# Optimization experiments

Measured on AMD Instinct MI355X. Metric: run time of the kernel, lower is better.

Reference implementation:

```python
import jax, jax.numpy as jnp
import numpy as np

INPUT_SIZE = (320, 320)   # (ih, iw) from Detector.input_size
CONF_THRESH = 0.5
NMS_THRESH = 0.4
CLASS_OFFSET = 1e4        # class-offset trick: boxes of different classes never overlap,
                          # making joint NMS identical to the original per-class loop


def setup_inputs():
    key = jax.random.key(0)
    k1, k2, k3, k4 = jax.random.split(key, 4)
    B, N, C = 4, 6300, 80
    cxcy = jax.random.uniform(k1, (B, N, 2), dtype=jnp.float32) * 320.0
    wh = jax.random.uniform(k2, (B, N, 2), dtype=jnp.float32) * 120.0 + 4.0
    obj = jax.random.uniform(k3, (B, N, 1), dtype=jnp.float32)
    cls = jax.random.uniform(k4, (B, N, C), dtype=jnp.float32)
    prediction = jnp.concatenate([cxcy, wh, obj, cls], axis=-1)  # [B, N, 85]
    return {"prediction": prediction, "fh": 720, "fw": 1280}


def _pairwise_iou(b):
    # b: [N, 4] as (x1, y1, x2, y2); same +1 / eps convention as bbox_iou
    x1, y1, x2, y2 = b[:, 0], b[:, 1], b[:, 2], b[:, 3]
    iw = jnp.clip(jnp.minimum(x2[:, None], x2[None, :]) - jnp.maximum(x1[:, None], x1[None, :]) + 1, 0)
    ih = jnp.clip(jnp.minimum(y2[:, None], y2[None, :]) - jnp.maximum(y1[:, None], y1[None, :]) + 1, 0)
    inter = iw * ih
    area = (x2 - x1 + 1) * (y2 - y1 + 1)
    return inter / (area[:, None] + area[None, :] - inter + 1e-16)


def _nms_image(pred):
    # pred: [N, 85]
    N = pred.shape[0]
    obj = pred[:, 4]
    valid = obj >= CONF_THRESH                      # conf_thresh filter (as mask)
    cx, cy, w, h = pred[:, 0], pred[:, 1], pred[:, 2], pred[:, 3]
    boxes = jnp.stack([cx - w / 2, cy - h / 2, cx + w / 2, cy + h / 2], axis=1)
    class_conf = jnp.max(pred[:, 5:], axis=1)
    class_pred = jnp.argmax(pred[:, 5:], axis=1)
    # offset boxes per class -> cross-class IoU is exactly 0
    oboxes = boxes + (class_pred.astype(boxes.dtype) * CLASS_OFFSET)[:, None]
    score = jnp.where(valid, obj, -jnp.inf)
    order = jnp.argsort(-score)                     # descending confidence
    iou = _pairwise_iou(oboxes[order])              # [N, N]
    vs = valid[order]
    idx = jnp.arange(N)

    def step(sup, i):
        k = vs[i] & (~sup[i])                       # box i survives -> it suppresses
        sup = sup | (k & (idx > i) & (iou[i] >= NMS_THRESH))
        return sup, k

    _, keep_sorted = jax.lax.scan(step, jnp.zeros(N, dtype=bool), idx)
    keep = jnp.zeros(N, dtype=bool).at[order].set(keep_sorted)
    det = jnp.concatenate(
        [boxes, obj[:, None], class_conf[:, None], class_pred.astype(boxes.dtype)[:, None]],
        axis=1,
    )  # [N, 7] = (x1, y1, x2, y2, obj_conf, class_score, class_pred)
    return det, keep


def _bbox_fit(det, fh, fw):
    # det: [B, N, 7]; fh, fw python ints (frame size); INPUT_SIZE = (ih, iw)
    ih, iw = INPUT_SIZE
    fdim = max(fh, fw)
    pad_x = max((fh * iw / ih - fw) / 2, 0) * iw / fdim
    pad_y = max((fw * ih / iw - fh) / 2, 0) * ih / fdim
    sx = fw / (iw - 2 * pad_x)
    sy = fh / (ih - 2 * pad_y)
    x1 = jnp.clip((det[..., 0] - pad_x) * sx, 0, fw)
    y1 = jnp.clip((det[..., 1] - pad_y) * sy, 0, fh)
    x2 = jnp.clip((det[..., 2] - pad_x) * sx, 0, fw)
    y2 = jnp.clip((det[..., 3] - pad_y) * sy, 0, fh)
    return jnp.concatenate([jnp.stack([x1, y1, x2, y2], axis=-1), det[..., 4:]], axis=-1)


def reference(prediction, fh, fw):
    det, keep = jax.vmap(_nms_image)(prediction)    # [B, N, 7], [B, N]
    det = _bbox_fit(det, fh, fw)
    return det, keep
```

## Files before the change

### kernel.cpp

```cpp
#include <hip/hip_runtime.h>
#include <limits.h>
#include <math.h>

#define BB 4
#define NN 6300
#define NCLS 80
#define NB (BB * NCLS)
#define PSTRIDE 85
#define CONF_TH 0.5f
#define NMS_TH 0.4f
#define CAP2 512


__global__ void __launch_bounds__(320) zero_kernel(int* __restrict__ cnt_ws) {
  cnt_ws[threadIdx.x] = 0;
}

__global__ void __launch_bounds__(256) prep_kernel(
    const float* __restrict__ pred,
    const int* __restrict__ fhp, const int* __restrict__ fwp,
    float* __restrict__ det_out,
    float* __restrict__ keep_out,
    int*   __restrict__ cnt_ws,
    float* __restrict__ rec_ws)
{
  int gid = blockIdx.x * blockDim.x + threadIdx.x;
  if (gid >= BB * NN) return;
  const float* p = pred + (long)gid * PSTRIDE;

  float cx = p[0], cy = p[1], w = p[2], h = p[3], obj = p[4];
  float x1 = cx - 0.5f * w;
  float y1 = cy - 0.5f * h;
  float x2 = cx + 0.5f * w;
  float y2 = cy + 0.5f * h;

  float cmax = p[5];
  int cidx = 0;
  for (int j = 1; j < NCLS; ++j) {
    float v = p[5 + j];
    if (v > cmax) { cmax = v; cidx = j; }
  }

  double fh = (double)fhp[0], fw = (double)fwp[0];
  const double ihd = 320.0, iwd = 320.0;
  double fdim = fmax(fh, fw);
  double pad_x_d = fmax((fh * iwd / ihd - fw) / 2.0, 0.0) * iwd / fdim;
  double pad_y_d = fmax((fw * ihd / iwd - fh) / 2.0, 0.0) * ihd / fdim;
  float sx = (float)(fw / (iwd - 2.0 * pad_x_d));
  float sy = (float)(fh / (ihd - 2.0 * pad_y_d));
  float px = (float)pad_x_d, py = (float)pad_y_d;
  float fwf = (float)fw, fhf = (float)fh;

  float* d = det_out + (long)gid * 7;
  d[0] = fminf(fmaxf((x1 - px) * sx, 0.0f), fwf);
  d[1] = fminf(fmaxf((y1 - py) * sy, 0.0f), fhf);
  d[2] = fminf(fmaxf((x2 - px) * sx, 0.0f), fwf);
  d[3] = fminf(fmaxf((y2 - py) * sy, 0.0f), fhf);
  d[4] = obj;
  d[5] = cmax;
  d[6] = (float)cidx;

  keep_out[gid] = 0.0f;

  if (obj >= CONF_TH) {
    int b = gid / NN;
    int n = gid - b * NN;
    int bucket = b * NCLS + cidx;
    int pos = atomicAdd(&cnt_ws[bucket], 1);
    if (pos < CAP2) {
      float off = (float)cidx * 10000.0f;
      float* r = rec_ws + ((size_t)bucket * CAP2 + pos) * 6;
      r[0] = x1 + off;
      r[1] = y1 + off;
      r[2] = x2 + off;
      r[3] = y2 + off;
      r[4] = obj;
      r[5] = __int_as_float(n);
    }
  }
}

__global__ void __launch_bounds__(256) nms_kernel(
    const int*   __restrict__ cnt_ws,
    const float* __restrict__ rec_ws,
    float* __restrict__ keep_out)
{
  const int tid = threadIdx.x;
  const int wv = tid >> 6;
  const int lane = tid & 63;
  const int bucket0 = blockIdx.x * 4;

  {
    const int bucket = bucket0 + wv;
    const int cnt = min(cnt_ws[bucket], CAP2);
    if (cnt > 0 && cnt <= 64) {
      float x1 = 0.f, y1 = 0.f, x2 = 0.f, y2 = 0.f;
      int n = 0;
      unsigned long long key;
      if (lane < cnt) {
        const float* r = rec_ws + ((size_t)bucket * CAP2 + lane) * 6;
        x1 = r[0]; y1 = r[1]; x2 = r[2]; y2 = r[3];
        float sc = r[4];
        n = __float_as_int(r[5]);
        key = ((unsigned long long)__float_as_uint(sc) << 32) |
              (unsigned)(0x7FFFFFFF - n);
      } else {
        key = (unsigned long long)lane;
      }
      int src = lane;

      for (int k = 2; k <= 64; k <<= 1) {
        for (int j = k >> 1; j > 0; j >>= 1) {
          unsigned long long ok = __shfl_xor(key, j);
          int osrc = __shfl_xor(src, j);
          bool lower = ((lane & j) == 0);
          bool asc = ((lane & k) != 0);
          bool mine_gt = key > ok;
          bool take = asc ? (lower ? mine_gt : !mine_gt)
                          : (lower ? !mine_gt : mine_gt);
          if (take) { key = ok; src = osrc; }
        }
      }

      float sx1 = __shfl(x1, src), sy1 = __shfl(y1, src);
      float sx2 = __shfl(x2, src), sy2 = __shfl(y2, src);
      int   sn  = __shfl(n, src);
      float area = __fmul_rn(__fadd_rn(__fsub_rn(sx2, sx1), 1.0f),
                             __fadd_rn(__fsub_rn(sy2, sy1), 1.0f));

      unsigned long long sup = 0ull;
      for (int i = 0; i < cnt; ++i) {
        if ((sup >> i) & 1ull) continue;
        float bx1 = __shfl(sx1, i), by1 = __shfl(sy1, i);
        float bx2 = __shfl(sx2, i), by2 = __shfl(sy2, i);
        float bar = __shfl(area, i);
        bool kill = false;
        if (lane > i && lane < cnt) {
          float iw_ = fmaxf(__fadd_rn(__fsub_rn(fminf(bx2, sx2),
                                                fmaxf(bx1, sx1)), 1.0f), 0.0f);
          float ih_ = fmaxf(__fadd_rn(__fsub_rn(fminf(by2, sy2),
                                                fmaxf(by1, sy1)), 1.0f), 0.0f);
          float inter = __fmul_rn(iw_, ih_);
          float denom = __fadd_rn(__fsub_rn(__fadd_rn(bar, area), inter), 1e-16f);
          kill = __fdiv_rn(inter, denom) >= NMS_TH;
        }
        sup |= __ballot(kill);
      }
      if (lane < cnt && !((sup >> lane) & 1ull)) {
        int b = bucket / NCLS;
        keep_out[b * NN + sn] = 1.0f;
      }
    }
  }

  __syncthreads();

  __shared__ float s_sc[CAP2];
  __shared__ float s_x1[CAP2], s_y1[CAP2], s_x2[CAP2], s_y2[CAP2];
  __shared__ int   s_idx[CAP2];
  __shared__ unsigned char s_sup[CAP2];

  for (int w2 = 0; w2 < 4; ++w2) {
    const int bucket = bucket0 + w2;
    const int cnt = min(cnt_ws[bucket], CAP2);
    if (cnt <= 64) continue;

    for (int i = tid; i < cnt; i += 256) {
      const float* r = rec_ws + ((size_t)bucket * CAP2 + i) * 6;
      s_x1[i] = r[0]; s_y1[i] = r[1]; s_x2[i] = r[2]; s_y2[i] = r[3];
      s_sc[i] = r[4]; s_idx[i] = __float_as_int(r[5]);
      s_sup[i] = 0;
    }
    __syncthreads();

    int M = 1;
    while (M < cnt) M <<= 1;
    for (int i = cnt + tid; i < M; i += 256) {
      s_sc[i] = -INFINITY; s_idx[i] = INT_MAX;
      s_x1[i] = 0.f; s_y1[i] = 0.f; s_x2[i] = 0.f; s_y2[i] = 0.f;
    }
    __syncthreads();

    for (int k = 2; k <= M; k <<= 1) {
      for (int j = k >> 1; j > 0; j >>= 1) {
        for (int i = tid; i < M; i += 256) {
          int ixj = i ^ j;
          if (ixj > i) {
            float si = s_sc[i], sj = s_sc[ixj];
            int ii = s_idx[i], ij = s_idx[ixj];
            bool before_ij = (si > sj) || (si == sj && ii < ij);
            bool before_ji = (sj > si) || (sj == si && ij < ii);
            bool up = ((i & k) == 0);
            bool dosw = up ? before_ji : before_ij;
            if (dosw) {
              s_sc[i] = sj;  s_sc[ixj] = si;
              s_idx[i] = ij; s_idx[ixj] = ii;
              float t;
              t = s_x1[i]; s_x1[i] = s_x1[ixj]; s_x1[ixj] = t;
              t = s_y1[i]; s_y1[i] = s_y1[ixj]; s_y1[ixj] = t;
              t = s_x2[i]; s_x2[i] = s_x2[ixj]; s_x2[ixj] = t;
              t = s_y2[i]; s_y2[i] = s_y2[ixj]; s_y2[ixj] = t;
            }
          }
        }
        __syncthreads();
      }
    }

    const int b = bucket / NCLS;
    for (int i = 0; i < cnt; ++i) {
      if (!s_sup[i]) {
        float x1i = s_x1[i], y1i = s_y1[i], x2i = s_x2[i], y2i = s_y2[i];
        float ai = __fmul_rn(__fadd_rn(__fsub_rn(x2i, x1i), 1.0f),
                             __fadd_rn(__fsub_rn(y2i, y1i), 1.0f));
        if (tid == 0) keep_out[b * NN + s_idx[i]] = 1.0f;
        for (int j = i + 1 + tid; j < cnt; j += 256) {
          float iw_ = fmaxf(__fadd_rn(__fsub_rn(fminf(x2i, s_x2[j]),
                                                fmaxf(x1i, s_x1[j])), 1.0f), 0.0f);
          float ih_ = fmaxf(__fadd_rn(__fsub_rn(fminf(y2i, s_y2[j]),
                                                fmaxf(y1i, s_y1[j])), 1.0f), 0.0f);
          float inter = __fmul_rn(iw_, ih_);
          float aj = __fmul_rn(__fadd_rn(__fsub_rn(s_x2[j], s_x1[j]), 1.0f),
                               __fadd_rn(__fsub_rn(s_y2[j], s_y1[j]), 1.0f));
          float denom = __fadd_rn(__fsub_rn(__fadd_rn(ai, aj), inter), 1e-16f);
          if (__fdiv_rn(inter, denom) >= NMS_TH) s_sup[j] = 1;
        }
      }
      __syncthreads();
    }
    __syncthreads();
  }
}

extern "C" void kernel_launch(void* const* d_in, const int* in_sizes, int n_in,
                              void* d_out, int out_size, void* d_ws, size_t ws_size,
                              hipStream_t stream) {
  const float* pred = (const float*)d_in[0];
  const int* fhp = (const int*)d_in[1];
  const int* fwp = (const int*)d_in[2];

  float* det_out  = (float*)d_out;
  float* keep_out = det_out + (size_t)BB * NN * 7;

  int*   cnt_ws = (int*)d_ws;
  float* rec_ws = (float*)((char*)d_ws + 4096);

  zero_kernel<<<1, NB, 0, stream>>>(cnt_ws);

  int nThreads = BB * NN;
  prep_kernel<<<(nThreads + 255) / 256, 256, 0, stream>>>(
      pred, fhp, fwp, det_out, keep_out, cnt_ws, rec_ws);

  nms_kernel<<<NB / 4, 256, 0, stream>>>(cnt_ws, rec_ws, keep_out);
}
```

Baseline: 84.50 us.

## Fuse zero, prep and NMS kernels into one launch with grid barriers

Replaces the three separate kernel launches (counter zeroing, box prep and bucketing, per-class NMS) with a single 99-block kernel. Block 0 clears the counters and publishes a magic flag that the other blocks wait on, and an atomic arrival counter acts as a grid barrier before the first 80 blocks run NMS. This removes two launch gaps and the inter-kernel idle time. In exchange it relies on all blocks being resident at the same time for the spin-waits. The flag is never reset between calls, so later invocations may start bucketing before block 0 has cleared the counters.

After: 95.25 us. 1.13x slower.

```diff
diff --git a/kernel.cpp b/kernel.cpp
--- a/kernel.cpp
+++ b/kernel.cpp
@@ -10,85 +10,113 @@
 #define CONF_TH 0.5f
 #define NMS_TH 0.4f
 #define CAP2 512
-
-
-__global__ void __launch_bounds__(320) zero_kernel(int* __restrict__ cnt_ws) {
-  cnt_ws[threadIdx.x] = 0;
-}
-
-__global__ void __launch_bounds__(256) prep_kernel(
+#define NBLK 99
+#define NMSBLK 80
+#define MAGIC 0x51D3C0DE
+
+
+__global__ void __launch_bounds__(256) fused_kernel(
     const float* __restrict__ pred,
     const int* __restrict__ fhp, const int* __restrict__ fwp,
     float* __restrict__ det_out,
     float* __restrict__ keep_out,
-    int*   __restrict__ cnt_ws,
+    int*   ctrl,
     float* __restrict__ rec_ws)
 {
-  int gid = blockIdx.x * blockDim.x + threadIdx.x;
-  if (gid >= BB * NN) return;
-  const float* p = pred + (long)gid * PSTRIDE;
-
-  float cx = p[0], cy = p[1], w = p[2], h = p[3], obj = p[4];
-  float x1 = cx - 0.5f * w;
-  float y1 = cy - 0.5f * h;
-  float x2 = cx + 0.5f * w;
-  float y2 = cy + 0.5f * h;
-
-  float cmax = p[5];
-  int cidx = 0;
-  for (int j = 1; j < NCLS; ++j) {
-    float v = p[5 + j];
-    if (v > cmax) { cmax = v; cidx = j; }
-  }
-
-  double fh = (double)fhp[0], fw = (double)fwp[0];
-  const double ihd = 320.0, iwd = 320.0;
-  double fdim = fmax(fh, fw);
-  double pad_x_d = fmax((fh * iwd / ihd - fw) / 2.0, 0.0) * iwd / fdim;
-  double pad_y_d = fmax((fw * ihd / iwd - fh) / 2.0, 0.0) * ihd / fdim;
-  float sx = (float)(fw / (iwd - 2.0 * pad_x_d));
-  float sy = (float)(fh / (ihd - 2.0 * pad_y_d));
-  float px = (float)pad_x_d, py = (float)pad_y_d;
-  float fwf = (float)fw, fhf = (float)fh;
-
-  float* d = det_out + (long)gid * 7;
-  d[0] = fminf(fmaxf((x1 - px) * sx, 0.0f), fwf);
-  d[1] = fminf(fmaxf((y1 - py) * sy, 0.0f), fhf);
-  d[2] = fminf(fmaxf((x2 - px) * sx, 0.0f), fwf);
-  d[3] = fminf(fmaxf((y2 - py) * sy, 0.0f), fhf);
-  d[4] = obj;
-  d[5] = cmax;
-  d[6] = (float)cidx;
-
-  keep_out[gid] = 0.0f;
-
-  if (obj >= CONF_TH) {
-    int b = gid / NN;
-    int n = gid - b * NN;
-    int bucket = b * NCLS + cidx;
-    int pos = atomicAdd(&cnt_ws[bucket], 1);
-    if (pos < CAP2) {
-      float off = (float)cidx * 10000.0f;
-      float* r = rec_ws + ((size_t)bucket * CAP2 + pos) * 6;
-      r[0] = x1 + off;
-      r[1] = y1 + off;
-      r[2] = x2 + off;
-      r[3] = y2 + off;
-      r[4] = obj;
-      r[5] = __int_as_float(n);
-    }
-  }
-}
-
-__global__ void __launch_bounds__(256) nms_kernel(
-    const int*   __restrict__ cnt_ws,
-    const float* __restrict__ rec_ws,
-    float* __restrict__ keep_out)
-{
   const int tid = threadIdx.x;
+  const int blk = blockIdx.x;
+  int* cnt_ws = ctrl;
+  int* arrive = ctrl + NB;
+  int* flag   = ctrl + NB + 1;
+
+  if (blk == 0) {
+    for (int i = tid; i < NB + 1; i += 256) ctrl[i] = 0;
+    __syncthreads();
+    if (tid == 0)
+      __hip_atomic_store(flag, (int)MAGIC, __ATOMIC_RELEASE,
+                         __HIP_MEMORY_SCOPE_AGENT);
+  } else {
+    if (tid == 0) {
+      while (__hip_atomic_load(flag, __ATOMIC_ACQUIRE,
+                               __HIP_MEMORY_SCOPE_AGENT) != (int)MAGIC)
+        __builtin_amdgcn_s_sleep(2);
+    }
+    __syncthreads();
+  }
+
+  const int gid = blk * 256 + tid;
+  if (gid < BB * NN) {
+    const float* p = pred + (long)gid * PSTRIDE;
+
+    float cx = p[0], cy = p[1], w = p[2], h = p[3], obj = p[4];
+    float x1 = cx - 0.5f * w;
+    float y1 = cy - 0.5f * h;
+    float x2 = cx + 0.5f * w;
+    float y2 = cy + 0.5f * h;
+
+    float cmax = p[5];
+    int cidx = 0;
+    for (int j = 1; j < NCLS; ++j) {
+      float v = p[5 + j];
+      if (v > cmax) { cmax = v; cidx = j; }
+    }
+
+    double fh = (double)fhp[0], fw = (double)fwp[0];
+    const double ihd = 320.0, iwd = 320.0;
+    double fdim = fmax(fh, fw);
+    double pad_x_d = fmax((fh * iwd / ihd - fw) / 2.0, 0.0) * iwd / fdim;
+    double pad_y_d = fmax((fw * ihd / iwd - fh) / 2.0, 0.0) * ihd / fdim;
+    float sx = (float)(fw / (iwd - 2.0 * pad_x_d));
+    float sy = (float)(fh / (ihd - 2.0 * pad_y_d));
+    float px = (float)pad_x_d, py = (float)pad_y_d;
+    float fwf = (float)fw, fhf = (float)fh;
+
+    float* d = det_out + (long)gid * 7;
+    d[0] = fminf(fmaxf((x1 - px) * sx, 0.0f), fwf);
+    d[1] = fminf(fmaxf((y1 - py) * sy, 0.0f), fhf);
+    d[2] = fminf(fmaxf((x2 - px) * sx, 0.0f), fwf);
+    d[3] = fminf(fmaxf((y2 - py) * sy, 0.0f), fhf);
+    d[4] = obj;
+    d[5] = cmax;
+    d[6] = (float)cidx;
+
+    keep_out[gid] = 0.0f;
+
+    if (obj >= CONF_TH) {
+      int b = gid / NN;
+      int n = gid - b * NN;
+      int bucket = b * NCLS + cidx;
+      int pos = atomicAdd(&cnt_ws[bucket], 1);
+      if (pos < CAP2) {
+        float off = (float)cidx * 10000.0f;
+        float* r = rec_ws + ((size_t)bucket * CAP2 + pos) * 6;
+        r[0] = x1 + off;
+        r[1] = y1 + off;
+        r[2] = x2 + off;
+        r[3] = y2 + off;
+        r[4] = obj;
+        r[5] = __int_as_float(n);
+      }
+    }
+  }
+
+  __syncthreads();
+  if (tid == 0) {
+    __threadfence();
+    atomicAdd(arrive, 1);
+  }
+  if (blk >= NMSBLK) return;
+  if (tid == 0) {
+    while (__hip_atomic_load(arrive, __ATOMIC_ACQUIRE,
+                             __HIP_MEMORY_SCOPE_AGENT) != NBLK)
+      __builtin_amdgcn_s_sleep(2);
+    __threadfence();
+  }
+  __syncthreads();
+
   const int wv = tid >> 6;
   const int lane = tid & 63;
-  const int bucket0 = blockIdx.x * 4;
+  const int bucket0 = blk * 4;
 
   {
     const int bucket = bucket0 + wv;
@@ -242,14 +270,9 @@
   float* det_out  = (float*)d_out;
   float* keep_out = det_out + (size_t)BB * NN * 7;
 
-  int*   cnt_ws = (int*)d_ws;
+  int*   ctrl   = (int*)d_ws;
   float* rec_ws = (float*)((char*)d_ws + 4096);
 
-  zero_kernel<<<1, NB, 0, stream>>>(cnt_ws);
-
-  int nThreads = BB * NN;
-  prep_kernel<<<(nThreads + 255) / 256, 256, 0, stream>>>(
-      pred, fhp, fwp, det_out, keep_out, cnt_ws, rec_ws);
-
-  nms_kernel<<<NB / 4, 256, 0, stream>>>(cnt_ws, rec_ws, keep_out);
+  fused_kernel<<<NBLK, 256, 0, stream>>>(
+      pred, fhp, fwp, det_out, keep_out, ctrl, rec_ws);
 }
```
